# Kernel optimization log

Hardware: AMD Instinct MI355X
Metric: run time of the kernel (lower is better)

The kernel has to match this reference:

```python
import jax, jax.numpy as jnp
import numpy as np

HIDDEN = 1024
NUM_HEAD = 16
HEAD_DIM = HIDDEN // NUM_HEAD
VOCAB = 32000
MAX_LEN = 1024
EMBED = 512
BATCH = 4
SEQ = MAX_LEN  # mask broadcasting requires seq == max_len


def setup_inputs() -> dict:
    key = jax.random.key(0)
    ks = jax.random.split(key, 12)
    std = 0.02
    inp = {
        'input_ids': jax.random.randint(ks[0], (BATCH, SEQ), 0, VOCAB),
        'W_word': jax.random.normal(ks[1], (VOCAB, EMBED), jnp.float32) * std,
        'W_pos': jax.random.normal(ks[2], (MAX_LEN, EMBED), jnp.float32) * std,
        'Wq': jax.random.normal(ks[3], (HIDDEN, HIDDEN), jnp.float32) * std,
        'Wk': jax.random.normal(ks[4], (HIDDEN, HIDDEN), jnp.float32) * std,
        'Wv': jax.random.normal(ks[5], (HIDDEN, HIDDEN), jnp.float32) * std,
        'Wo': jax.random.normal(ks[6], (HIDDEN, HIDDEN), jnp.float32) * std,
        'W1': jax.random.normal(ks[7], (4 * HIDDEN, HIDDEN), jnp.float32) * std,
        'W2': jax.random.normal(ks[8], (HIDDEN, 4 * HIDDEN), jnp.float32) * std,
        'W_eh': jax.random.normal(ks[9], (HIDDEN, EMBED), jnp.float32) * std,
        'W_he': jax.random.normal(ks[10], (EMBED, HIDDEN), jnp.float32) * std,
        'W_lm': jax.random.normal(ks[11], (VOCAB, EMBED), jnp.float32) * std,
    }
    return inp


def reference(input_ids, W_word, W_pos, Wq, Wk, Wv, Wo, W1, W2, W_eh, W_he, W_lm):
    B, S = input_ids.shape
    # embeddings
    h = W_word[input_ids] + W_pos[jnp.arange(S)][None, :, :]  # [B,S,E]
    h = h @ W_eh.T  # embed -> hidden, [B,S,H]
    residual = h
    # QKV projections (Linear with weight [out,in]: y = x @ W.T)
    q = (h @ Wq.T).reshape(B, S, NUM_HEAD, HEAD_DIM).transpose(0, 2, 1, 3)
    k = (h @ Wk.T).reshape(B, S, NUM_HEAD, HEAD_DIM).transpose(0, 2, 1, 3)
    v = (h @ Wv.T).reshape(B, S, NUM_HEAD, HEAD_DIM).transpose(0, 2, 1, 3)
    # note: original scales by sqrt(hidden_size), NOT sqrt(head_dim)
    scores = jnp.einsum('bhqd,bhkd->bhqk', q, k) / jnp.sqrt(jnp.float32(HIDDEN))
    mask = jnp.tril(jnp.ones((S, S), dtype=bool))[None, None]
    scores = jnp.where(mask, scores, jnp.finfo(jnp.float32).min)
    attn = jax.nn.softmax(scores.astype(jnp.float32), axis=-1)
    out = jnp.einsum('bhqk,bhkd->bhqd', attn, v)
    out = out.transpose(0, 2, 1, 3).reshape(B, S, HIDDEN)
    h = residual + out @ Wo.T
    # MLP
    residual = h
    x = jax.nn.relu(h @ W1.T)
    h = residual + x @ W2.T
    # hidden -> embed, lm head
    h = h @ W_he.T
    logits = h @ W_lm.T  # [B,S,VOCAB]
    return logits
```

## Files before the change

### kernel.cpp

```cpp
#include <hip/hip_runtime.h>
#include <hip/hip_bf16.h>

#define HIDDEN 1024
#define NHEAD 16
#define HDIM 64
#define VOCAB 32000
#define SEQLEN 1024
#define EMBED 512
#define BATCH 4
#define ROWS (BATCH*SEQLEN)

typedef __bf16 bf16x8 __attribute__((ext_vector_type(8)));
typedef float f32x4 __attribute__((ext_vector_type(4)));
typedef unsigned short u16;

#define MFMA(a_, b_, c_) __builtin_amdgcn_mfma_f32_16x16x32_bf16(a_, b_, c_, 0, 0, 0)

#define VMCNT4 asm volatile("s_waitcnt vmcnt(4)" ::: "memory")
#define VMCNT0 asm volatile("s_waitcnt vmcnt(0)" ::: "memory")
#define LGKM0  asm volatile("s_waitcnt lgkmcnt(0)" ::: "memory")
#define CFENCE asm volatile("" ::: "memory")
#define SBAR   __builtin_amdgcn_s_barrier()
#define SCHEDB __builtin_amdgcn_sched_barrier(0)

__device__ __forceinline__ u16 f2bf(float f) {
  unsigned u = __builtin_bit_cast(unsigned, f);
  u = u + 0x7FFFu + ((u >> 16) & 1u);
  return (u16)(u >> 16);
}

#define GLDS(g_, l_) __builtin_amdgcn_global_load_lds( \
    (const __attribute__((address_space(1))) void*)(g_), \
    (__attribute__((address_space(3))) void*)(l_), 16, 0, 0)

struct Prep {
  const float* src[8]; u16* dst[8];
  const float* wlm; u16* wlm_dst;
  const int* ids; const float* wword; const float* wpos; u16* h0b;
};
__global__ void prep_kernel(Prep pp) {
  int b = blockIdx.x;
  if (b < 13312) {
    int seg, off;
    if (b < 4096)        { seg = b >> 10; off = b & 1023; }
    else if (b < 8192)   { seg = 4; off = b - 4096; }
    else if (b < 12288)  { seg = 5; off = b - 8192; }
    else if (b < 12800)  { seg = 6; off = b - 12288; }
    else                 { seg = 7; off = b - 12800; }
    size_t i = ((size_t)off * 256 + threadIdx.x) * 4;
    float4 v = *(const float4*)(pp.src[seg] + i);
    unsigned a = f2bf(v.x) | ((unsigned)f2bf(v.y) << 16);
    unsigned d = f2bf(v.z) | ((unsigned)f2bf(v.w) << 16);
    *(uint2*)(pp.dst[seg] + i) = make_uint2(a, d);
  } else if (b < 29312) {
    if (!pp.wlm_dst) return;
    int off = b - 13312;
    size_t i = ((size_t)off * 256 + threadIdx.x) * 4;
    float4 v = *(const float4*)(pp.wlm + i);
    unsigned a = f2bf(v.x) | ((unsigned)f2bf(v.y) << 16);
    unsigned d = f2bf(v.z) | ((unsigned)f2bf(v.w) << 16);
    *(uint2*)(pp.wlm_dst + i) = make_uint2(a, d);
  } else {
    int off = b - 29312;
    int row = off * 2 + (threadIdx.x >> 7);
    int e = (threadIdx.x & 127) * 4;
    int s = row & (SEQLEN - 1);
    int id = pp.ids[row];
    float4 a = *(const float4*)(pp.wword + (size_t)id * EMBED + e);
    float4 c = *(const float4*)(pp.wpos + (size_t)s * EMBED + e);
    unsigned lo = f2bf(a.x + c.x) | ((unsigned)f2bf(a.y + c.y) << 16);
    unsigned hi = f2bf(a.z + c.z) | ((unsigned)f2bf(a.w + c.w) << 16);
    *(uint2*)(pp.h0b + (size_t)row * EMBED + e) = make_uint2(lo, hi);
  }
}

template<int EPI, bool WF32, bool WB16, bool BF32, bool SWZ, bool NT = false>
__global__ __launch_bounds__(256, 2) void gemm128(
    const u16* __restrict__ A, const u16* __restrict__ Bb,
    const float* __restrict__ Bf,
    float* __restrict__ C, u16* __restrict__ Cb,
    const float* __restrict__ R, int K, int ldc)
{
  __shared__ u16 As[2][128 * 64];
  __shared__ u16 Bs[2][128 * 64];
  int tid = threadIdx.x;
  int lane = tid & 63, wave = tid >> 6;
  int wr = wave >> 1, wc = wave & 1;
  int cl = lane & 15, gp = (lane >> 4) & 3;

  int bx = blockIdx.x, by = blockIdx.y;
  if (SWZ) {
    int nwg = gridDim.x * gridDim.y;
    int flat = by * gridDim.x + bx;
    int cpx = nwg >> 3;
    int swz = (flat & 7) * cpx + (flat >> 3);
    bx = swz % gridDim.x; by = swz / gridDim.x;
  }
  int m0 = bx * 128, n0 = by * 128;

  int srow8 = lane >> 3;
  int scol = (((lane & 7) - srow8) & 7) * 8;
  int pos0 = ((gp + cl) & 7) * 8;
  int pos1 = ((gp + cl + 4) & 7) * 8;

  f32x4 acc[4][4] = {};
  int nk = K >> 6;

  #pragma unroll
  for (int i = 0; i < 4; ++i) {
    int c = i * 4 + wave;
    GLDS(A + (size_t)(m0 + c * 8 + srow8) * K + scol, &As[0][c * 512]);
  }
  if (!BF32) {
    #pragma unroll
    for (int i = 0; i < 4; ++i) {
      int c = i * 4 + wave;
      GLDS(Bb + (size_t)(n0 + c * 8 + srow8) * K + scol, &Bs[0][c * 512]);
    }
  } else {
    #pragma unroll
    for (int it = 0; it < 4; ++it) {
      int idx = it * 256 + tid;
      int row = idx >> 3, p = idx & 7;
      int gc = (p - row) & 7;
      const float* src = Bf + (size_t)(n0 + row) * K + gc * 8;
      float4 v0 = *(const float4*)src, v1 = *(const float4*)(src + 4);
      union { bf16x8 v; u16 s[8]; } u;
      u.s[0]=f2bf(v0.x); u.s[1]=f2bf(v0.y); u.s[2]=f2bf(v0.z); u.s[3]=f2bf(v0.w);
      u.s[4]=f2bf(v1.x); u.s[5]=f2bf(v1.y); u.s[6]=f2bf(v1.z); u.s[7]=f2bf(v1.w);
      *(bf16x8*)&Bs[0][row * 64 + p * 8] = u.v;
    }
  }

  for (int kt = 0; kt < nk; ++kt) {
    int buf = kt & 1;
    int kb = (kt + 1) << 6;
    bool more = kt + 1 < nk;

    if (more) {
      #pragma unroll
      for (int i = 0; i < 4; ++i) {
        int c = i * 4 + wave;
        GLDS(A + (size_t)(m0 + c * 8 + srow8) * K + kb + scol, &As[buf ^ 1][c * 512]);
      }
    }
    if (BF32) { VMCNT0; } else if (more) { VMCNT4; } else { VMCNT0; }
    SCHEDB;
    SBAR;
    CFENCE; SCHEDB;

    bf16x8 af[4][2], bfv[4][2];
    #pragma unroll
    for (int n = 0; n < 4; ++n) {
      int r = (wc * 64 + n * 16 + cl) * 64;
      bfv[n][0] = *(const bf16x8*)&Bs[buf][r + pos0];
      bfv[n][1] = *(const bf16x8*)&Bs[buf][r + pos1];
    }
    #pragma unroll
    for (int m = 0; m < 4; ++m) {
      int r = (wr * 64 + m * 16 + cl) * 64;
      af[m][0] = *(const bf16x8*)&As[buf][r + pos0];
      af[m][1] = *(const bf16x8*)&As[buf][r + pos1];
    }

    __builtin_amdgcn_s_setprio(1);
    #pragma unroll
    for (int m = 0; m < 2; ++m)
      #pragma unroll
      for (int n = 0; n < 4; ++n)
        #pragma unroll
        for (int ks = 0; ks < 2; ++ks)
          acc[m][n] = MFMA(af[m][ks], bfv[n][ks], acc[m][n]);
    __builtin_amdgcn_s_setprio(0);

    if (more) {
      if (!BF32) {
        #pragma unroll
        for (int i = 0; i < 4; ++i) {
          int c = i * 4 + wave;
          GLDS(Bb + (size_t)(n0 + c * 8 + srow8) * K + kb + scol, &Bs[buf ^ 1][c * 512]);
        }
      } else {
        #pragma unroll
        for (int it = 0; it < 4; ++it) {
          int idx = it * 256 + tid;
          int row = idx >> 3, p = idx & 7;
          int gc = (p - row) & 7;
          const float* src = Bf + (size_t)(n0 + row) * K + kb + gc * 8;
          float4 v0 = *(const float4*)src, v1 = *(const float4*)(src + 4);
          union { bf16x8 v; u16 s[8]; } u;
          u.s[0]=f2bf(v0.x); u.s[1]=f2bf(v0.y); u.s[2]=f2bf(v0.z); u.s[3]=f2bf(v0.w);
          u.s[4]=f2bf(v1.x); u.s[5]=f2bf(v1.y); u.s[6]=f2bf(v1.z); u.s[7]=f2bf(v1.w);
          *(bf16x8*)&Bs[buf ^ 1][row * 64 + p * 8] = u.v;
        }
      }
    }

    __builtin_amdgcn_s_setprio(1);
    #pragma unroll
    for (int n = 0; n < 4; ++n)
      #pragma unroll
      for (int ks = 0; ks < 2; ++ks)
        acc[2][n] = MFMA(af[2][ks], bfv[n][ks], acc[2][n]);
    __builtin_amdgcn_s_setprio(0);

    LGKM0;
    SCHEDB;
    SBAR;
    CFENCE; SCHEDB;

    __builtin_amdgcn_s_setprio(1);
    #pragma unroll
    for (int n = 0; n < 4; ++n)
      #pragma unroll
      for (int ks = 0; ks < 2; ++ks)
        acc[3][n] = MFMA(af[3][ks], bfv[n][ks], acc[3][n]);
    __builtin_amdgcn_s_setprio(0);
  }

  int r0 = gp * 4;
  #pragma unroll
  for (int m = 0; m < 4; ++m) {
    #pragma unroll
    for (int n = 0; n < 4; ++n) {
      int col = n0 + wc * 64 + n * 16 + cl;
      #pragma unroll
      for (int j = 0; j < 4; ++j) {
        int row = m0 + wr * 64 + m * 16 + r0 + j;
        float v = acc[m][n][j];
        if (EPI == 1) v += R[(size_t)row * ldc + col];
        if (EPI == 2) v = fmaxf(v, 0.f);
        if (WF32) {
          if (NT) __builtin_nontemporal_store(v, &C[(size_t)row * ldc + col]);
          else C[(size_t)row * ldc + col] = v;
        }
        if (WB16) Cb[(size_t)row * ldc + col] = f2bf(v);
      }
    }
  }
}

template<int EPI, bool WF32, bool WB16, bool SWZ, bool NT = false>
__global__ __launch_bounds__(512) void gemm256(
    const u16* __restrict__ A, const u16* __restrict__ B,
    float* __restrict__ C, u16* __restrict__ Cb,
    const float* __restrict__ R, int K, int ldc)
{
  __shared__ __align__(16) u16 smem[4][256 * 64];
  int tid = threadIdx.x;
  int lane = tid & 63, wave = tid >> 6;
  int wr = wave >> 2, wc = wave & 3;
  int cl = lane & 15, gp = (lane >> 4) & 3;

  int bx = blockIdx.x, by = blockIdx.y;
  if (SWZ) {
    int nwg = gridDim.x * gridDim.y;
    int flat = by * gridDim.x + bx;
    int cpx = nwg >> 3;
    int swz = (flat & 7) * cpx + (flat >> 3);
    bx = swz % gridDim.x; by = swz / gridDim.x;
  }
  int m0 = bx * 256, n0 = by * 256;

  int srow8 = lane >> 3;
  int scol = (((lane & 7) - srow8) & 7) * 8;
  int pos0 = ((gp + cl) & 7) * 8;
  int pos1 = ((gp + cl + 4) & 7) * 8;

  f32x4 acc[8][4] = {};
  int nk = K >> 6;

  #pragma unroll
  for (int i = 0; i < 4; ++i) {
    int c = i * 8 + wave;
    GLDS(A + (size_t)(m0 + c * 8 + srow8) * K + scol, &smem[0][c * 512]);
  }
  #pragma unroll
  for (int i = 0; i < 4; ++i) {
    int c = i * 8 + wave;
    GLDS(B + (size_t)(n0 + c * 8 + srow8) * K + scol, &smem[2][c * 512]);
  }

  for (int kt = 0; kt < nk; ++kt) {
    int buf = kt & 1;
    int kb = (kt + 1) << 6;
    bool more = kt + 1 < nk;

    if (more) {
      #pragma unroll
      for (int i = 0; i < 4; ++i) {
        int c = i * 8 + wave;
        GLDS(A + (size_t)(m0 + c * 8 + srow8) * K + kb + scol, &smem[buf ^ 1][c * 512]);
      }
      VMCNT4;
    } else {
      VMCNT0;
    }
    SCHEDB;
    SBAR;
    CFENCE; SCHEDB;

    bf16x8 af0[4][2], af1[4][2], bf0[2][2], bf1[2][2];
    #pragma unroll
    for (int n = 0; n < 2; ++n) {
      int r = (wc * 64 + n * 16 + cl) * 64;
      bf0[n][0] = *(const bf16x8*)&smem[2 + buf][r + pos0];
      bf0[n][1] = *(const bf16x8*)&smem[2 + buf][r + pos1];
    }
    #pragma unroll
    for (int m = 0; m < 4; ++m) {
      int r = (wr * 128 + m * 16 + cl) * 64;
      af0[m][0] = *(const bf16x8*)&smem[buf][r + pos0];
      af0[m][1] = *(const bf16x8*)&smem[buf][r + pos1];
    }
    #pragma unroll
    for (int n = 0; n < 2; ++n) {
      int r = (wc * 64 + (n + 2) * 16 + cl) * 64;
      bf1[n][0] = *(const bf16x8*)&smem[2 + buf][r + pos0];
      bf1[n][1] = *(const bf16x8*)&smem[2 + buf][r + pos1];
    }
    #pragma unroll
    for (int m = 0; m < 4; ++m) {
      int r = (wr * 128 + (m + 4) * 16 + cl) * 64;
      af1[m][0] = *(const bf16x8*)&smem[buf][r + pos0];
      af1[m][1] = *(const bf16x8*)&smem[buf][r + pos1];
    }

    __builtin_amdgcn_s_setprio(1);
    #pragma unroll
    for (int m = 0; m < 4; ++m)
      #pragma unroll
      for (int n = 0; n < 2; ++n)
        #pragma unroll
        for (int ks = 0; ks < 2; ++ks)
          acc[m][n] = MFMA(af0[m][ks], bf0[n][ks], acc[m][n]);
    __builtin_amdgcn_s_setprio(0);

    if (more) {
      #pragma unroll
      for (int i = 0; i < 4; ++i) {
        int c = i * 8 + wave;
        GLDS(B + (size_t)(n0 + c * 8 + srow8) * K + kb + scol, &smem[2 + (buf ^ 1)][c * 512]);
      }
    }

    __builtin_amdgcn_s_setprio(1);
    #pragma unroll
    for (int m = 0; m < 4; ++m)
      #pragma unroll
      for (int n = 0; n < 2; ++n)
        #pragma unroll
        for (int ks = 0; ks < 2; ++ks)
          acc[m][n + 2] = MFMA(af0[m][ks], bf1[n][ks], acc[m][n + 2]);
    __builtin_amdgcn_s_setprio(0);

    LGKM0;
    SCHEDB;
    SBAR;
    CFENCE; SCHEDB;

    __builtin_amdgcn_s_setprio(1);
    #pragma unroll
    for (int m = 0; m < 4; ++m)
      #pragma unroll
      for (int n = 0; n < 2; ++n)
        #pragma unroll
        for (int ks = 0; ks < 2; ++ks)
          acc[m + 4][n] = MFMA(af1[m][ks], bf0[n][ks], acc[m + 4][n]);
    #pragma unroll
    for (int m = 0; m < 4; ++m)
      #pragma unroll
      for (int n = 0; n < 2; ++n)
        #pragma unroll
        for (int ks = 0; ks < 2; ++ks)
          acc[m + 4][n + 2] = MFMA(af1[m][ks], bf1[n][ks], acc[m + 4][n + 2]);
    __builtin_amdgcn_s_setprio(0);
  }

  if (WF32 && !WB16) {
    float* Cst = (float*)&smem[0][0];
    __syncthreads();
    #pragma unroll
    for (int g = 0; g < 4; ++g) {
      if ((g >> 1) == wr) {
        #pragma unroll
        for (int k = 0; k < 4; ++k) {
          int ar = (g & 1) * 4 + k;
          int rl = ar * 16 + gp * 4 - (g & 1) * 64;
          #pragma unroll
          for (int n = 0; n < 4; ++n) {
            int col = wc * 64 + n * 16 + cl;
            #pragma unroll
            for (int j = 0; j < 4; ++j)
              Cst[(rl + j) * 260 + col] = acc[ar][n][j];
          }
        }
      }
      __syncthreads();
      #pragma unroll
      for (int p = 0; p < 8; ++p) {
        int r = p * 8 + wave;
        int c4 = lane * 4;
        int grow = m0 + g * 64 + r;
        f32x4 v = *(f32x4*)&Cst[r * 260 + c4];
        if (EPI == 1) {
          f32x4 rv = *(const f32x4*)&R[(size_t)grow * ldc + n0 + c4];
          v = v + rv;
        }
        if (EPI == 2) {
          #pragma unroll
          for (int j = 0; j < 4; ++j) v[j] = fmaxf(v[j], 0.f);
        }
        if (NT) __builtin_nontemporal_store(v, (f32x4*)&C[(size_t)grow * ldc + n0 + c4]);
        else *(f32x4*)&C[(size_t)grow * ldc + n0 + c4] = v;
      }
      __syncthreads();
    }
  } else {
    int r0 = gp * 4;
    #pragma unroll
    for (int m = 0; m < 8; ++m) {
      #pragma unroll
      for (int n = 0; n < 4; ++n) {
        int col = n0 + wc * 64 + n * 16 + cl;
        #pragma unroll
        for (int j = 0; j < 4; ++j) {
          int row = m0 + wr * 128 + m * 16 + r0 + j;
          float v = acc[m][n][j];
          if (EPI == 1) v += R[(size_t)row * ldc + col];
          if (EPI == 2) v = fmaxf(v, 0.f);
          if (WF32) C[(size_t)row * ldc + col] = v;
          if (WB16) Cb[(size_t)row * ldc + col] = f2bf(v);
        }
      }
    }
  }
}

#define LSTR 72
__global__ __launch_bounds__(256) void attn_kernel(const u16* __restrict__ qkv,
                                                   u16* __restrict__ outb) {
  __shared__ u16 Ksm[2][64 * 64];
  __shared__ u16 Vsm[2][64 * LSTR];
  __shared__ u16 Psm[64 * LSTR];
  int qb = blockIdx.x, h = blockIdx.y, b = blockIdx.z;
  int tid = threadIdx.x;
  int lane = tid & 63, wave = tid >> 6;
  int cl = lane & 15, gp = lane >> 4;
  int srow8 = lane >> 3;
  int gsrc = (((lane & 7) - srow8) & 7) * 8;

  const u16* base = qkv + (size_t)b * SEQLEN * (3 * HIDDEN);

  int qrow_a = qb * 64 + wave * 16 + cl;
  const u16* qp = base + (size_t)qrow_a * (3 * HIDDEN) + h * HDIM;
  bf16x8 qf0 = *(const bf16x8*)(qp + gp * 8);
  bf16x8 qf1 = *(const bf16x8*)(qp + 32 + gp * 8);

  ushort4 vr[4];

  auto stageK = [&](int t, int bb) {
    #pragma unroll
    for (int i = 0; i < 2; ++i) {
      int c = wave * 2 + i;
      int row = c * 8 + srow8;
      GLDS(base + (size_t)(t * 64 + row) * (3 * HIDDEN) + HIDDEN + h * HDIM + gsrc,
           &Ksm[bb][c * 512]);
    }
  };
  auto loadV = [&](int t) {
    #pragma unroll
    for (int it = 0; it < 4; ++it) {
      int idx = it * 256 + tid;
      int row = idx >> 4, c4 = (idx & 15) * 4;
      vr[it] = *(const ushort4*)(base + (size_t)(t * 64 + row) * (3 * HIDDEN) +
                                 2 * HIDDEN + h * HDIM + c4);
    }
  };
  auto writeV = [&](int bb) {
    #pragma unroll
    for (int it = 0; it < 4; ++it) {
      int idx = it * 256 + tid;
      int row = idx >> 4, c4 = (idx & 15) * 4;
      Vsm[bb][(c4 + 0) * LSTR + row] = vr[it].x;
      Vsm[bb][(c4 + 1) * LSTR + row] = vr[it].y;
      Vsm[bb][(c4 + 2) * LSTR + row] = vr[it].z;
      Vsm[bb][(c4 + 3) * LSTR + row] = vr[it].w;
    }
  };

  stageK(0, 0);
  loadV(0);
  writeV(0);
  __syncthreads();

  float mrow[4], lrow[4];
  f32x4 oacc[4] = {};
  #pragma unroll
  for (int j = 0; j < 4; ++j) { mrow[j] = -INFINITY; lrow[j] = 0.f; }

  for (int t = 0; t <= qb; ++t) {
    int buf = t & 1;
    bool more = t < qb;
    if (more) { stageK(t + 1, buf ^ 1); loadV(t + 1); }

    f32x4 sfr[4];
    __builtin_amdgcn_s_setprio(1);
    #pragma unroll
    for (int n = 0; n < 4; ++n) {
      f32x4 z = {};
      bf16x8 kf0 = *(const bf16x8*)&Ksm[buf][(n * 16 + cl) * 64 + ((gp + cl) & 7) * 8];
      bf16x8 kf1 = *(const bf16x8*)&Ksm[buf][(n * 16 + cl) * 64 + ((gp + cl + 4) & 7) * 8];
      z = MFMA(qf0, kf0, z);
      z = MFMA(qf1, kf1, z);
      sfr[n] = z;
    }
    __builtin_amdgcn_s_setprio(0);

    #pragma unroll
    for (int n = 0; n < 4; ++n)
      #pragma unroll
      for (int j = 0; j < 4; ++j) {
        int qg = qb * 64 + wave * 16 + gp * 4 + j;
        int kg = t * 64 + n * 16 + cl;
        float sv = sfr[n][j] * 0.03125f;
        sfr[n][j] = (kg <= qg) ? sv : -1e30f;
      }
    float so[4];
    #pragma unroll
    for (int j = 0; j < 4; ++j) {
      float tm = fmaxf(fmaxf(sfr[0][j], sfr[1][j]), fmaxf(sfr[2][j], sfr[3][j]));
      tm = fmaxf(tm, __shfl_xor(tm, 1));
      tm = fmaxf(tm, __shfl_xor(tm, 2));
      tm = fmaxf(tm, __shfl_xor(tm, 4));
      tm = fmaxf(tm, __shfl_xor(tm, 8));
      float mn = fmaxf(mrow[j], tm);
      so[j] = __expf(mrow[j] - mn);
      mrow[j] = mn;
      float ts = 0.f;
      #pragma unroll
      for (int n = 0; n < 4; ++n) {
        float p = __expf(sfr[n][j] - mn);
        sfr[n][j] = p;
        ts += p;
      }
      ts += __shfl_xor(ts, 1); ts += __shfl_xor(ts, 2);
      ts += __shfl_xor(ts, 4); ts += __shfl_xor(ts, 8);
      lrow[j] = lrow[j] * so[j] + ts;
    }
    #pragma unroll
    for (int n = 0; n < 4; ++n)
      #pragma unroll
      for (int j = 0; j < 4; ++j)
        oacc[n][j] *= so[j];

    if (more) writeV(buf ^ 1);

    #pragma unroll
    for (int n = 0; n < 4; ++n)
      #pragma unroll
      for (int j = 0; j < 4; ++j)
        Psm[(wave * 16 + gp * 4 + j) * LSTR + n * 16 + cl] = f2bf(sfr[n][j]);
    __builtin_amdgcn_sched_barrier(0);

    bf16x8 pa0 = *(const bf16x8*)&Psm[(wave * 16 + cl) * LSTR + gp * 8];
    bf16x8 pa1 = *(const bf16x8*)&Psm[(wave * 16 + cl) * LSTR + 32 + gp * 8];
    __builtin_amdgcn_s_setprio(1);
    #pragma unroll
    for (int n = 0; n < 4; ++n) {
      bf16x8 vb0 = *(const bf16x8*)&Vsm[buf][(n * 16 + cl) * LSTR + gp * 8];
      bf16x8 vb1 = *(const bf16x8*)&Vsm[buf][(n * 16 + cl) * LSTR + 32 + gp * 8];
      oacc[n] = MFMA(pa0, vb0, oacc[n]);
      oacc[n] = MFMA(pa1, vb1, oacc[n]);
    }
    __builtin_amdgcn_s_setprio(0);

    __syncthreads();
  }

  #pragma unroll
  for (int n = 0; n < 4; ++n)
    #pragma unroll
    for (int j = 0; j < 4; ++j) {
      int qg = qb * 64 + wave * 16 + gp * 4 + j;
      int d = n * 16 + cl;
      outb[(size_t)(b * SEQLEN + qg) * HIDDEN + h * HDIM + d] = f2bf(oacc[n][j] / lrow[j]);
    }
}

extern "C" void kernel_launch(void* const* d_in, const int* in_sizes, int n_in,
                              void* d_out, int out_size, void* d_ws, size_t ws_size,
                              hipStream_t stream) {
  const int*   ids    = (const int*)d_in[0];
  const float* W_word = (const float*)d_in[1];
  const float* W_pos  = (const float*)d_in[2];
  const float* Wq     = (const float*)d_in[3];
  const float* Wk     = (const float*)d_in[4];
  const float* Wv     = (const float*)d_in[5];
  const float* Wo     = (const float*)d_in[6];
  const float* W1     = (const float*)d_in[7];
  const float* W2     = (const float*)d_in[8];
  const float* W_eh   = (const float*)d_in[9];
  const float* W_he   = (const float*)d_in[10];
  const float* W_lm   = (const float*)d_in[11];
  float* out = (float*)d_out;
  char*  ob  = (char*)d_out;
  char*  wb  = (char*)d_ws;

  const size_t MB = 1024 * 1024;
  float* h1    = (float*)(ob + 0 * MB);
  float* h2    = (float*)(ob + 16 * MB);
  u16*   h0b   = (u16*)(ob + 32 * MB);
  u16*   h1b   = (u16*)(ob + 36 * MB);
  u16*   qkvb  = (u16*)(ob + 44 * MB);
  u16*   attnb = (u16*)(ob + 68 * MB);
  u16*   h2b   = (u16*)(ob + 76 * MB);
  u16*   xb    = (u16*)(ob + 84 * MB);
  u16*   h3b   = (u16*)(ob + 116 * MB);
  u16*   Wqkv_b= (u16*)(ob + 124 * MB);
  u16*   Wo_b  = (u16*)(ob + 130 * MB);
  u16*   W1_b  = (u16*)(ob + 132 * MB);
  u16*   W2_b  = (u16*)(ob + 140 * MB);
  u16*   Weh_b = (u16*)(ob + 148 * MB);
  u16*   Whe_b = (u16*)(ob + 149 * MB);
  u16*   he_b  = (u16*)(wb + 0);
  u16*   Wlm_b = (u16*)(wb + 4 * MB);
  bool big_ws = ws_size >= 36 * MB;

  Prep pp;
  pp.src[0] = Wq;  pp.dst[0] = Wqkv_b + 0 * 1024 * 1024;
  pp.src[1] = Wk;  pp.dst[1] = Wqkv_b + 1 * 1024 * 1024;
  pp.src[2] = Wv;  pp.dst[2] = Wqkv_b + 2 * 1024 * 1024;
  pp.src[3] = Wo;  pp.dst[3] = Wo_b;
  pp.src[4] = W1;  pp.dst[4] = W1_b;
  pp.src[5] = W2;  pp.dst[5] = W2_b;
  pp.src[6] = W_eh; pp.dst[6] = Weh_b;
  pp.src[7] = W_he; pp.dst[7] = Whe_b;
  pp.wlm = W_lm; pp.wlm_dst = big_ws ? Wlm_b : nullptr;
  pp.ids = ids; pp.wword = W_word; pp.wpos = W_pos; pp.h0b = h0b;
  prep_kernel<<<dim3(31360), 256, 0, stream>>>(pp);

  gemm128<0, true, true, false, false><<<dim3(32, 8), 256, 0, stream>>>(
      h0b, Weh_b, nullptr, h1, h1b, nullptr, 512, HIDDEN);
  gemm128<0, false, true, false, false><<<dim3(32, 24), 256, 0, stream>>>(
      h1b, Wqkv_b, nullptr, nullptr, qkvb, nullptr, 1024, 3 * HIDDEN);
  attn_kernel<<<dim3(16, 16, 4), 256, 0, stream>>>(qkvb, attnb);
  gemm128<1, true, true, false, false><<<dim3(32, 8), 256, 0, stream>>>(
      attnb, Wo_b, nullptr, h2, h2b, h1, 1024, HIDDEN);
  gemm256<2, false, true, false><<<dim3(16, 16), 512, 0, stream>>>(
      h2b, W1_b, nullptr, xb, nullptr, 1024, 4 * HIDDEN);
  gemm128<1, false, true, false, false><<<dim3(32, 8), 256, 0, stream>>>(
      xb, W2_b, nullptr, nullptr, h3b, h2, 4096, HIDDEN);
  gemm128<0, false, true, false, false><<<dim3(32, 4), 256, 0, stream>>>(
      h3b, Whe_b, nullptr, nullptr, he_b, nullptr, 1024, EMBED);
  if (big_ws)
    gemm256<0, true, false, true, true><<<dim3(16, 125), 512, 0, stream>>>(
        he_b, Wlm_b, out, nullptr, nullptr, 512, VOCAB);
  else
    gemm128<0, true, false, true, true, true><<<dim3(32, 250), 256, 0, stream>>>(
        he_b, nullptr, W_lm, out, nullptr, nullptr, 512, VOCAB);
}
```

Before: 495.3 us.

## Drop 256-tile GEMM, use templated BN gemm128 with narrower tiles for small-N GEMMs

Makes the 128-row GEMM generic in N tile width (BN=64 or 128) and removes the 256x256 gemm256 kernel. The N=1024 and N=512 GEMMs now use 128x64 tiles so more workgroups fill the CUs, and the W1 and LM-head GEMMs switch to 128x128 tiles. An LDS-staged, coalesced fp32 epilogue is added to gemm128 for the LM-head output. Smaller tiles trade lower per-tile data reuse for better occupancy and wave balance.

```diff
diff --git a/kernel.cpp b/kernel.cpp
--- a/kernel.cpp
+++ b/kernel.cpp
@@ -74,15 +74,21 @@
   }
 }
 
-template<int EPI, bool WF32, bool WB16, bool BF32, bool SWZ, bool NT = false>
+template<int EPI, bool WF32, bool WB16, bool BF32, bool SWZ, bool NT, int BN>
 __global__ __launch_bounds__(256, 2) void gemm128(
     const u16* __restrict__ A, const u16* __restrict__ Bb,
     const float* __restrict__ Bf,
     float* __restrict__ C, u16* __restrict__ Cb,
     const float* __restrict__ R, int K, int ldc)
 {
-  __shared__ u16 As[2][128 * 64];
-  __shared__ u16 Bs[2][128 * 64];
+  constexpr int NF  = BN / 32;
+  constexpr int BCH = BN / 32;
+  __shared__ __align__(16) u16 smem[16384 + 2 * BN * 64];
+  u16* As0 = &smem[0];
+  u16* As1 = &smem[8192];
+  u16* Bs0 = &smem[16384];
+  u16* Bs1 = &smem[16384 + BN * 64];
+
   int tid = threadIdx.x;
   int lane = tid & 63, wave = tid >> 6;
   int wr = wave >> 1, wc = wave & 1;
@@ -96,30 +102,30 @@
     int swz = (flat & 7) * cpx + (flat >> 3);
     bx = swz % gridDim.x; by = swz / gridDim.x;
   }
-  int m0 = bx * 128, n0 = by * 128;
+  int m0 = bx * 128, n0 = by * BN;
 
   int srow8 = lane >> 3;
   int scol = (((lane & 7) - srow8) & 7) * 8;
   int pos0 = ((gp + cl) & 7) * 8;
   int pos1 = ((gp + cl + 4) & 7) * 8;
 
-  f32x4 acc[4][4] = {};
+  f32x4 acc[4][NF] = {};
   int nk = K >> 6;
 
   #pragma unroll
   for (int i = 0; i < 4; ++i) {
     int c = i * 4 + wave;
-    GLDS(A + (size_t)(m0 + c * 8 + srow8) * K + scol, &As[0][c * 512]);
+    GLDS(A + (size_t)(m0 + c * 8 + srow8) * K + scol, As0 + c * 512);
   }
   if (!BF32) {
     #pragma unroll
-    for (int i = 0; i < 4; ++i) {
+    for (int i = 0; i < BCH; ++i) {
       int c = i * 4 + wave;
-      GLDS(Bb + (size_t)(n0 + c * 8 + srow8) * K + scol, &Bs[0][c * 512]);
+      GLDS(Bb + (size_t)(n0 + c * 8 + srow8) * K + scol, Bs0 + c * 512);
     }
   } else {
     #pragma unroll
-    for (int it = 0; it < 4; ++it) {
+    for (int it = 0; it < BN / 32; ++it) {
       int idx = it * 256 + tid;
       int row = idx >> 3, p = idx & 7;
       int gc = (p - row) & 7;
@@ -128,12 +134,16 @@
       union { bf16x8 v; u16 s[8]; } u;
       u.s[0]=f2bf(v0.x); u.s[1]=f2bf(v0.y); u.s[2]=f2bf(v0.z); u.s[3]=f2bf(v0.w);
       u.s[4]=f2bf(v1.x); u.s[5]=f2bf(v1.y); u.s[6]=f2bf(v1.z); u.s[7]=f2bf(v1.w);
-      *(bf16x8*)&Bs[0][row * 64 + p * 8] = u.v;
+      *(bf16x8*)&Bs0[row * 64 + p * 8] = u.v;
     }
   }
 
   for (int kt = 0; kt < nk; ++kt) {
     int buf = kt & 1;
+    u16* Asb = buf ? As1 : As0;
+    u16* Bsb = buf ? Bs1 : Bs0;
+    u16* Asn = buf ? As0 : As1;
+    u16* Bsn = buf ? Bs0 : Bs1;
     int kb = (kt + 1) << 6;
     bool more = kt + 1 < nk;
 
@@ -141,7 +151,7 @@
       #pragma unroll
       for (int i = 0; i < 4; ++i) {
         int c = i * 4 + wave;
-        GLDS(A + (size_t)(m0 + c * 8 + srow8) * K + kb + scol, &As[buf ^ 1][c * 512]);
+        GLDS(A + (size_t)(m0 + c * 8 + srow8) * K + kb + scol, Asn + c * 512);
       }
     }
     if (BF32) { VMCNT0; } else if (more) { VMCNT4; } else { VMCNT0; }
@@ -149,25 +159,25 @@
     SBAR;
     CFENCE; SCHEDB;
 
-    bf16x8 af[4][2], bfv[4][2];
-    #pragma unroll
-    for (int n = 0; n < 4; ++n) {
-      int r = (wc * 64 + n * 16 + cl) * 64;
-      bfv[n][0] = *(const bf16x8*)&Bs[buf][r + pos0];
-      bfv[n][1] = *(const bf16x8*)&Bs[buf][r + pos1];
+    bf16x8 af[4][2], bfv[NF][2];
+    #pragma unroll
+    for (int n = 0; n < NF; ++n) {
+      int r = (wc * (BN / 2) + n * 16 + cl) * 64;
+      bfv[n][0] = *(const bf16x8*)&Bsb[r + pos0];
+      bfv[n][1] = *(const bf16x8*)&Bsb[r + pos1];
     }
     #pragma unroll
     for (int m = 0; m < 4; ++m) {
       int r = (wr * 64 + m * 16 + cl) * 64;
-      af[m][0] = *(const bf16x8*)&As[buf][r + pos0];
-      af[m][1] = *(const bf16x8*)&As[buf][r + pos1];
+      af[m][0] = *(const bf16x8*)&Asb[r + pos0];
+      af[m][1] = *(const bf16x8*)&Asb[r + pos1];
     }
 
     __builtin_amdgcn_s_setprio(1);
     #pragma unroll
     for (int m = 0; m < 2; ++m)
       #pragma unroll
-      for (int n = 0; n < 4; ++n)
+      for (int n = 0; n < NF; ++n)
         #pragma unroll
         for (int ks = 0; ks < 2; ++ks)
           acc[m][n] = MFMA(af[m][ks], bfv[n][ks], acc[m][n]);
@@ -176,13 +186,13 @@
     if (more) {
       if (!BF32) {
         #pragma unroll
-        for (int i = 0; i < 4; ++i) {
+        for (int i = 0; i < BCH; ++i) {
           int c = i * 4 + wave;
-          GLDS(Bb + (size_t)(n0 + c * 8 + srow8) * K + kb + scol, &Bs[buf ^ 1][c * 512]);
+          GLDS(Bb + (size_t)(n0 + c * 8 + srow8) * K + kb + scol, Bsn + c * 512);
         }
       } else {
         #pragma unroll
-        for (int it = 0; it < 4; ++it) {
+        for (int it = 0; it < BN / 32; ++it) {
           int idx = it * 256 + tid;
           int row = idx >> 3, p = idx & 7;
           int gc = (p - row) & 7;
@@ -191,14 +201,14 @@
           union { bf16x8 v; u16 s[8]; } u;
           u.s[0]=f2bf(v0.x); u.s[1]=f2bf(v0.y); u.s[2]=f2bf(v0.z); u.s[3]=f2bf(v0.w);
           u.s[4]=f2bf(v1.x); u.s[5]=f2bf(v1.y); u.s[6]=f2bf(v1.z); u.s[7]=f2bf(v1.w);
-          *(bf16x8*)&Bs[buf ^ 1][row * 64 + p * 8] = u.v;
+          *(bf16x8*)&Bsn[row * 64 + p * 8] = u.v;
         }
       }
     }
 
     __builtin_amdgcn_s_setprio(1);
     #pragma unroll
-    for (int n = 0; n < 4; ++n)
+    for (int n = 0; n < NF; ++n)
       #pragma unroll
       for (int ks = 0; ks < 2; ++ks)
         acc[2][n] = MFMA(af[2][ks], bfv[n][ks], acc[2][n]);
@@ -211,221 +221,54 @@
 
     __builtin_amdgcn_s_setprio(1);
     #pragma unroll
-    for (int n = 0; n < 4; ++n)
+    for (int n = 0; n < NF; ++n)
       #pragma unroll
       for (int ks = 0; ks < 2; ++ks)
         acc[3][n] = MFMA(af[3][ks], bfv[n][ks], acc[3][n]);
     __builtin_amdgcn_s_setprio(0);
   }
 
-  int r0 = gp * 4;
-  #pragma unroll
-  for (int m = 0; m < 4; ++m) {
-    #pragma unroll
-    for (int n = 0; n < 4; ++n) {
-      int col = n0 + wc * 64 + n * 16 + cl;
-      #pragma unroll
-      for (int j = 0; j < 4; ++j) {
-        int row = m0 + wr * 64 + m * 16 + r0 + j;
-        float v = acc[m][n][j];
-        if (EPI == 1) v += R[(size_t)row * ldc + col];
-        if (EPI == 2) v = fmaxf(v, 0.f);
-        if (WF32) {
-          if (NT) __builtin_nontemporal_store(v, &C[(size_t)row * ldc + col]);
-          else C[(size_t)row * ldc + col] = v;
-        }
-        if (WB16) Cb[(size_t)row * ldc + col] = f2bf(v);
-      }
-    }
-  }
-}
-
-template<int EPI, bool WF32, bool WB16, bool SWZ, bool NT = false>
-__global__ __launch_bounds__(512) void gemm256(
-    const u16* __restrict__ A, const u16* __restrict__ B,
-    float* __restrict__ C, u16* __restrict__ Cb,
-    const float* __restrict__ R, int K, int ldc)
-{
-  __shared__ __align__(16) u16 smem[4][256 * 64];
-  int tid = threadIdx.x;
-  int lane = tid & 63, wave = tid >> 6;
-  int wr = wave >> 2, wc = wave & 3;
-  int cl = lane & 15, gp = (lane >> 4) & 3;
-
-  int bx = blockIdx.x, by = blockIdx.y;
-  if (SWZ) {
-    int nwg = gridDim.x * gridDim.y;
-    int flat = by * gridDim.x + bx;
-    int cpx = nwg >> 3;
-    int swz = (flat & 7) * cpx + (flat >> 3);
-    bx = swz % gridDim.x; by = swz / gridDim.x;
-  }
-  int m0 = bx * 256, n0 = by * 256;
-
-  int srow8 = lane >> 3;
-  int scol = (((lane & 7) - srow8) & 7) * 8;
-  int pos0 = ((gp + cl) & 7) * 8;
-  int pos1 = ((gp + cl + 4) & 7) * 8;
-
-  f32x4 acc[8][4] = {};
-  int nk = K >> 6;
-
-  #pragma unroll
-  for (int i = 0; i < 4; ++i) {
-    int c = i * 8 + wave;
-    GLDS(A + (size_t)(m0 + c * 8 + srow8) * K + scol, &smem[0][c * 512]);
-  }
-  #pragma unroll
-  for (int i = 0; i < 4; ++i) {
-    int c = i * 8 + wave;
-    GLDS(B + (size_t)(n0 + c * 8 + srow8) * K + scol, &smem[2][c * 512]);
-  }
-
-  for (int kt = 0; kt < nk; ++kt) {
-    int buf = kt & 1;
-    int kb = (kt + 1) << 6;
-    bool more = kt + 1 < nk;
-
-    if (more) {
-      #pragma unroll
-      for (int i = 0; i < 4; ++i) {
-        int c = i * 8 + wave;
-        GLDS(A + (size_t)(m0 + c * 8 + srow8) * K + kb + scol, &smem[buf ^ 1][c * 512]);
-      }
-      VMCNT4;
-    } else {
-      VMCNT0;
-    }
-    SCHEDB;
-    SBAR;
-    CFENCE; SCHEDB;
-
-    bf16x8 af0[4][2], af1[4][2], bf0[2][2], bf1[2][2];
-    #pragma unroll
-    for (int n = 0; n < 2; ++n) {
-      int r = (wc * 64 + n * 16 + cl) * 64;
-      bf0[n][0] = *(const bf16x8*)&smem[2 + buf][r + pos0];
-      bf0[n][1] = *(const bf16x8*)&smem[2 + buf][r + pos1];
-    }
-    #pragma unroll
-    for (int m = 0; m < 4; ++m) {
-      int r = (wr * 128 + m * 16 + cl) * 64;
-      af0[m][0] = *(const bf16x8*)&smem[buf][r + pos0];
-      af0[m][1] = *(const bf16x8*)&smem[buf][r + pos1];
-    }
-    #pragma unroll
-    for (int n = 0; n < 2; ++n) {
-      int r = (wc * 64 + (n + 2) * 16 + cl) * 64;
-      bf1[n][0] = *(const bf16x8*)&smem[2 + buf][r + pos0];
-      bf1[n][1] = *(const bf16x8*)&smem[2 + buf][r + pos1];
-    }
-    #pragma unroll
-    for (int m = 0; m < 4; ++m) {
-      int r = (wr * 128 + (m + 4) * 16 + cl) * 64;
-      af1[m][0] = *(const bf16x8*)&smem[buf][r + pos0];
-      af1[m][1] = *(const bf16x8*)&smem[buf][r + pos1];
-    }
-
-    __builtin_amdgcn_s_setprio(1);
-    #pragma unroll
-    for (int m = 0; m < 4; ++m)
-      #pragma unroll
-      for (int n = 0; n < 2; ++n)
+  if constexpr (WF32 && !WB16 && BN == 128) {
+    float* Cst = (float*)&smem[0];
+    __syncthreads();
+    #pragma unroll
+    for (int g = 0; g < 2; ++g) {
+      if (wr == g) {
         #pragma unroll
-        for (int ks = 0; ks < 2; ++ks)
-          acc[m][n] = MFMA(af0[m][ks], bf0[n][ks], acc[m][n]);
-    __builtin_amdgcn_s_setprio(0);
-
-    if (more) {
-      #pragma unroll
-      for (int i = 0; i < 4; ++i) {
-        int c = i * 8 + wave;
-        GLDS(B + (size_t)(n0 + c * 8 + srow8) * K + kb + scol, &smem[2 + (buf ^ 1)][c * 512]);
-      }
-    }
-
-    __builtin_amdgcn_s_setprio(1);
-    #pragma unroll
-    for (int m = 0; m < 4; ++m)
-      #pragma unroll
-      for (int n = 0; n < 2; ++n)
-        #pragma unroll
-        for (int ks = 0; ks < 2; ++ks)
-          acc[m][n + 2] = MFMA(af0[m][ks], bf1[n][ks], acc[m][n + 2]);
-    __builtin_amdgcn_s_setprio(0);
-
-    LGKM0;
-    SCHEDB;
-    SBAR;
-    CFENCE; SCHEDB;
-
-    __builtin_amdgcn_s_setprio(1);
-    #pragma unroll
-    for (int m = 0; m < 4; ++m)
-      #pragma unroll
-      for (int n = 0; n < 2; ++n)
-        #pragma unroll
-        for (int ks = 0; ks < 2; ++ks)
-          acc[m + 4][n] = MFMA(af1[m][ks], bf0[n][ks], acc[m + 4][n]);
-    #pragma unroll
-    for (int m = 0; m < 4; ++m)
-      #pragma unroll
-      for (int n = 0; n < 2; ++n)
-        #pragma unroll
-        for (int ks = 0; ks < 2; ++ks)
-          acc[m + 4][n + 2] = MFMA(af1[m][ks], bf1[n][ks], acc[m + 4][n + 2]);
-    __builtin_amdgcn_s_setprio(0);
-  }
-
-  if (WF32 && !WB16) {
-    float* Cst = (float*)&smem[0][0];
-    __syncthreads();
-    #pragma unroll
-    for (int g = 0; g < 4; ++g) {
-      if ((g >> 1) == wr) {
-        #pragma unroll
-        for (int k = 0; k < 4; ++k) {
-          int ar = (g & 1) * 4 + k;
-          int rl = ar * 16 + gp * 4 - (g & 1) * 64;
+        for (int m = 0; m < 4; ++m)
           #pragma unroll
-          for (int n = 0; n < 4; ++n) {
-            int col = wc * 64 + n * 16 + cl;
+          for (int n = 0; n < 4; ++n)
             #pragma unroll
             for (int j = 0; j < 4; ++j)
-              Cst[(rl + j) * 260 + col] = acc[ar][n][j];
-          }
-        }
+              Cst[(m * 16 + gp * 4 + j) * 132 + wc * 64 + n * 16 + cl] = acc[m][n][j];
       }
       __syncthreads();
+      int r2 = lane >> 5, cw = lane & 31;
       #pragma unroll
       for (int p = 0; p < 8; ++p) {
-        int r = p * 8 + wave;
-        int c4 = lane * 4;
+        int r = p * 8 + wave * 2 + r2;
         int grow = m0 + g * 64 + r;
-        f32x4 v = *(f32x4*)&Cst[r * 260 + c4];
-        if (EPI == 1) {
-          f32x4 rv = *(const f32x4*)&R[(size_t)grow * ldc + n0 + c4];
-          v = v + rv;
-        }
+        f32x4 v = *(f32x4*)&Cst[r * 132 + cw * 4];
+        if (EPI == 1) v = v + *(const f32x4*)&R[(size_t)grow * ldc + n0 + cw * 4];
         if (EPI == 2) {
           #pragma unroll
           for (int j = 0; j < 4; ++j) v[j] = fmaxf(v[j], 0.f);
         }
-        if (NT) __builtin_nontemporal_store(v, (f32x4*)&C[(size_t)grow * ldc + n0 + c4]);
-        else *(f32x4*)&C[(size_t)grow * ldc + n0 + c4] = v;
+        if (NT) __builtin_nontemporal_store(v, (f32x4*)&C[(size_t)grow * ldc + n0 + cw * 4]);
+        else *(f32x4*)&C[(size_t)grow * ldc + n0 + cw * 4] = v;
       }
       __syncthreads();
     }
   } else {
     int r0 = gp * 4;
     #pragma unroll
-    for (int m = 0; m < 8; ++m) {
-      #pragma unroll
-      for (int n = 0; n < 4; ++n) {
-        int col = n0 + wc * 64 + n * 16 + cl;
+    for (int m = 0; m < 4; ++m) {
+      #pragma unroll
+      for (int n = 0; n < NF; ++n) {
+        int col = n0 + wc * (BN / 2) + n * 16 + cl;
         #pragma unroll
         for (int j = 0; j < 4; ++j) {
-          int row = m0 + wr * 128 + m * 16 + r0 + j;
+          int row = m0 + wr * 64 + m * 16 + r0 + j;
           float v = acc[m][n][j];
           if (EPI == 1) v += R[(size_t)row * ldc + col];
           if (EPI == 2) v = fmaxf(v, 0.f);
@@ -640,23 +483,23 @@
   pp.ids = ids; pp.wword = W_word; pp.wpos = W_pos; pp.h0b = h0b;
   prep_kernel<<<dim3(31360), 256, 0, stream>>>(pp);
 
-  gemm128<0, true, true, false, false><<<dim3(32, 8), 256, 0, stream>>>(
+  gemm128<0, true, true, false, false, false, 64><<<dim3(32, 16), 256, 0, stream>>>(
       h0b, Weh_b, nullptr, h1, h1b, nullptr, 512, HIDDEN);
-  gemm128<0, false, true, false, false><<<dim3(32, 24), 256, 0, stream>>>(
+  gemm128<0, false, true, false, false, false, 128><<<dim3(32, 24), 256, 0, stream>>>(
       h1b, Wqkv_b, nullptr, nullptr, qkvb, nullptr, 1024, 3 * HIDDEN);
   attn_kernel<<<dim3(16, 16, 4), 256, 0, stream>>>(qkvb, attnb);
-  gemm128<1, true, true, false, false><<<dim3(32, 8), 256, 0, stream>>>(
+  gemm128<1, true, true, false, false, false, 64><<<dim3(32, 16), 256, 0, stream>>>(
       attnb, Wo_b, nullptr, h2, h2b, h1, 1024, HIDDEN);
-  gemm256<2, false, true, false><<<dim3(16, 16), 512, 0, stream>>>(
-      h2b, W1_b, nullptr, xb, nullptr, 1024, 4 * HIDDEN);
-  gemm128<1, false, true, false, false><<<dim3(32, 8), 256, 0, stream>>>(
+  gemm128<2, false, true, false, false, false, 128><<<dim3(32, 32), 256, 0, stream>>>(
+      h2b, W1_b, nullptr, nullptr, xb, nullptr, 1024, 4 * HIDDEN);
+  gemm128<1, false, true, false, false, false, 64><<<dim3(32, 16), 256, 0, stream>>>(
       xb, W2_b, nullptr, nullptr, h3b, h2, 4096, HIDDEN);
-  gemm128<0, false, true, false, false><<<dim3(32, 4), 256, 0, stream>>>(
+  gemm128<0, false, true, false, false, false, 64><<<dim3(32, 8), 256, 0, stream>>>(
       h3b, Whe_b, nullptr, nullptr, he_b, nullptr, 1024, EMBED);
   if (big_ws)
-    gemm256<0, true, false, true, true><<<dim3(16, 125), 512, 0, stream>>>(
-        he_b, Wlm_b, out, nullptr, nullptr, 512, VOCAB);
+    gemm128<0, true, false, false, true, true, 128><<<dim3(32, 250), 256, 0, stream>>>(
+        he_b, Wlm_b, nullptr, out, nullptr, nullptr, 512, VOCAB);
   else
-    gemm128<0, true, false, true, true, true><<<dim3(32, 250), 256, 0, stream>>>(
+    gemm128<0, true, false, true, true, true, 128><<<dim3(32, 250), 256, 0, stream>>>(
         he_b, nullptr, W_lm, out, nullptr, nullptr, 512, VOCAB);
 }
```

Measured after the change: 502.9 us. No clear change (+1.5%).
